# Optimization experiments

Measured on AMD Instinct MI355X. Metric: run time of the kernel, lower is better.

The kernel has to match this reference:

```python
import jax, jax.numpy as jnp
import numpy as np
from jax import lax

H = 1024  # hidden_size
L = 2     # num_layers


def gru_cell(x, h, Wih, Whh, bih, bhh):
    # PyTorch GRU gate order: r, z, n
    gi = x @ Wih.T + bih          # [B, 3H]
    gh = h @ Whh.T + bhh          # [B, 3H]
    ir, iz, inn = jnp.split(gi, 3, axis=-1)
    hr, hz, hn = jnp.split(gh, 3, axis=-1)
    r = jax.nn.sigmoid(ir + hr)
    z = jax.nn.sigmoid(iz + hz)
    n = jnp.tanh(inn + r * hn)
    return (1.0 - z) * n + z * h


def stacked_step(h, x_t, layers):
    # h: [L, B, H]; x_t: [B, in]; layers: list of (Wih, Whh, bih, bhh)
    hs = []
    inp = x_t
    for l, (Wih, Whh, bih, bhh) in enumerate(layers):
        hl = gru_cell(inp, h[l], Wih, Whh, bih, bhh)
        hs.append(hl)
        inp = hl
    return jnp.stack(hs), inp  # new hidden stack, top-layer output


def run_gru_seq(x_seq, h0, layers):
    # x_seq: [B, S, in] -> scan over time
    def step(h, x_t):
        h_new, out = stacked_step(h, x_t, layers)
        return h_new, out
    h_final, outs = lax.scan(step, h0, jnp.transpose(x_seq, (1, 0, 2)))
    return outs[-1], h_final  # last-timestep top-layer output [B, H]


def setup_inputs() -> dict:
    key = jax.random.key(0)
    ks = jax.random.split(key, 10)
    B, S = 128, 256

    def xavier(k, shape):
        fan_out, fan_in = shape
        std = np.sqrt(2.0 / (fan_in + fan_out))
        return jax.random.normal(k, shape, dtype=jnp.float32) * std

    inp = {
        "x": jax.random.normal(ks[0], (B, S), dtype=jnp.float32),
        "h0": jax.random.uniform(ks[1], (L, B, H), dtype=jnp.float32) * 0.01,
        "Wih0": xavier(ks[2], (3 * H, 1)),
        "Whh0": xavier(ks[3], (3 * H, H)),
        "bih0": jnp.zeros((3 * H,), jnp.float32),
        "bhh0": jnp.zeros((3 * H,), jnp.float32),
        "Wih1": xavier(ks[4], (3 * H, H)),
        "Whh1": xavier(ks[5], (3 * H, H)),
        "bih1": jnp.zeros((3 * H,), jnp.float32),
        "bhh1": jnp.zeros((3 * H,), jnp.float32),
        "fc_w": jax.random.uniform(ks[6], (1, H), jnp.float32, -1.0 / np.sqrt(H), 1.0 / np.sqrt(H)),
        "fc_b": jax.random.uniform(ks[7], (1,), jnp.float32, -1.0 / np.sqrt(H), 1.0 / np.sqrt(H)),
        "forcast_length": 8,
    }
    return inp


def reference(x, h0, Wih0, Whh0, bih0, bhh0, Wih1, Whh1, bih1, bhh1, fc_w, fc_b, forcast_length):
    layers = [(Wih0, Whh0, bih0, bhh0), (Wih1, Whh1, bih1, bhh1)]

    # forecast step i=0: full conditioning sequence
    out0, h = run_gru_seq(x[..., None], h0, layers)   # [B, H], [L, B, H]
    y0 = out0 @ fc_w.T + fc_b                          # [B, 1]

    def fstep(carry, _):
        xc, hc = carry                                 # xc: [B, 1]
        h_new, out = stacked_step(hc, xc, layers)
        y = out @ fc_w.T + fc_b                        # [B, 1]
        return (y, h_new), y[:, 0]

    (y_last, h_final), ys = lax.scan(fstep, (y0, h), None, length=forcast_length - 1)
    forcast_out = jnp.concatenate([y0[:, 0][None, :], ys], axis=0)  # [F, B]
    return jnp.mean(forcast_out, axis=0), h_final
```

## Files before the change

### kernel.cpp

```cpp
#include <hip/hip_runtime.h>

#define NB 128
#define NH 1024
#define NS 256
#define NF 8
#define NBLK 192
#define NTH 512
#define AG  __HIP_MEMORY_SCOPE_AGENT

#define GLOBL 0
#define RELL  64
#define INITL 128
#define XCNT  192
#define XARR  512
#define XCPY  1024

typedef _Float16 half_t;
typedef _Float16 f16x8 __attribute__((ext_vector_type(8)));
typedef float f32x4 __attribute__((ext_vector_type(4)));
typedef unsigned long long u64;

struct GP {
    const float *x, *hin, *Wih0, *Whh0, *bih0, *bhh0, *Wih1, *Whh1, *bih1, *bhh1, *fcw, *fcb;
    float *gib0, *gib1, *ypart, *out;
    half_t *h0b0, *h0b1, *h1b0, *h1b1;
    char *reg;
    unsigned *bar;
};

__device__ __forceinline__ float fast_sigmoid(float x) { return 1.0f / (1.0f + __expf(-x)); }
__device__ __forceinline__ float fast_tanh(float x) {
    float e = __expf(2.0f * x);
    return (e - 1.0f) / (e + 1.0f);
}

__device__ __forceinline__ u64 ldu64(const void* p) {
    return __hip_atomic_load((const u64*)p, __ATOMIC_RELAXED, AG);
}
__device__ __forceinline__ void stu64(void* p, u64 v) {
    __hip_atomic_store((u64*)p, v, __ATOMIC_RELAXED, AG);
}
__device__ __forceinline__ float ldf32(const float* p) {
    return __hip_atomic_load(p, __ATOMIC_RELAXED, AG);
}
__device__ __forceinline__ void stf32(float* p, float v) {
    __hip_atomic_store(p, v, __ATOMIC_RELAXED, AG);
}
__device__ __forceinline__ unsigned aadd(unsigned* p, unsigned v) {
    return __hip_atomic_fetch_add(p, v, __ATOMIC_RELAXED, AG);
}
__device__ __forceinline__ unsigned ald(const unsigned* p) {
    return __hip_atomic_load(p, __ATOMIC_RELAXED, AG);
}

__device__ __forceinline__ void l2add(unsigned* p, unsigned v) {
    asm volatile("global_atomic_add %0, %1, off" :: "v"(p), "v"(v) : "memory");
}
__device__ __forceinline__ unsigned l2add_rtn(unsigned* p, unsigned v) {
    unsigned ret;
    asm volatile("global_atomic_add %0, %1, %2, off sc0\n\ts_waitcnt vmcnt(0)"
                 : "=v"(ret) : "v"(p), "v"(v) : "memory");
    return ret;
}

__global__ void k_init(const float* __restrict__ hin, half_t* __restrict__ h0h,
                       half_t* __restrict__ h1h) {
    int i = blockIdx.x * 256 + threadIdx.x;
    h0h[i] = (half_t)hin[i];
    h1h[i] = (half_t)hin[NB * NH + i];
}

__global__ __launch_bounds__(NTH)
void k_gru(GP p) {
    extern __shared__ char lds[];
    const int tid = threadIdx.x;
    const int l   = tid & 63;
    const int wv  = tid >> 6;
    const int bid = blockIdx.x;
    const int role = (bid < 64) ? 0 : (bid < 128 ? 1 : 2);
    const int bc   = bid & 63;
    const int colbase = bc * 16;
    float* hl  = (float*)(lds + 98304);
    int* meta  = (int*)(lds + 106496);
    unsigned* bar = p.bar;

    {
        const float* Wsrc = (role == 0) ? p.Whh0 : ((role == 1) ? p.Wih1 : p.Whh1);
        for (int i = tid; i < 12288; i += NTH) {
            int row = i >> 8, j = i & 255;
            int g = row >> 4, r = row & 15;
            float4 v = *(const float4*)(Wsrc + (size_t)(g * NH + colbase + r) * NH + j * 4);
            union { half_t h[4]; uint2 u; } cv;
            cv.h[0] = (half_t)v.x; cv.h[1] = (half_t)v.y;
            cv.h[2] = (half_t)v.z; cv.h[3] = (half_t)v.w;
            *(uint2*)(lds + (row * 2048 + ((j * 8) ^ ((row & 7) << 4)))) = cv.u;
        }
        if (role != 1) {
            const float* hsrc = p.hin + (role == 2 ? NB * NH : 0);
            for (int i = tid; i < NB * 16; i += NTH) {
                int b = i >> 4, cl = i & 15;
                hl[i] = hsrc[(size_t)b * NH + colbase + cl];
            }
        }
    }

    if (tid == 0) {
        unsigned x;
        asm volatile("s_getreg_b32 %0, hwreg(HW_REG_XCC_ID)" : "=s"(x));
        x &= 7;
        unsigned r = aadd(bar + XCNT + x * 32, 1u);
        asm volatile("s_waitcnt vmcnt(0)" ::: "memory");
        aadd(bar + INITL, 1u);
        while (ald(bar + INITL) < NBLK) __builtin_amdgcn_s_sleep(1);
        int nn = 0, cnt = 0;
        for (int k = 0; k < 8; ++k) {
            unsigned c = ald(bar + XCNT + k * 32);
            if (c) ++cnt;
            if (k == (int)x) nn = (int)c;
        }
        meta[0] = (int)x; meta[1] = (int)r; meta[2] = nn; meta[3] = cnt;
    }
    __syncthreads();
    const int xcd_  = meta[0];
    const int rank_ = meta[1];
    const int n_    = meta[2];
    const int nx_   = meta[3];

    const int cloc = l & 15;
    const int c = colbase + cloc;
    float bi_[3] = {0,0,0}, bh_[3] = {0,0,0}, wx_[3] = {0,0,0}, fcwv = 0.f, fcb_ = 0.f;
    if (role == 0) {
        #pragma unroll
        for (int g = 0; g < 3; ++g) {
            bi_[g] = p.bih0[g * NH + c]; bh_[g] = p.bhh0[g * NH + c];
            wx_[g] = p.Wih0[g * NH + c];
        }
        fcb_ = p.fcb[0];
    } else if (role == 2) {
        #pragma unroll
        for (int g = 0; g < 3; ++g) {
            bi_[g] = p.bih1[g * NH + c]; bh_[g] = p.bhh1[g * NH + c];
        }
        fcwv = p.fcw[c];
    }

    const int rbase[3] = { cloc * 2048, (16 + cloc) * 2048, (32 + cloc) * 2048 };
    const int rmask = (cloc & 7) << 4;
    const int kb0 = (l >> 4) << 4;
    const int arow = wv * 16 + cloc;
    const int b0base = wv * 16 + ((l >> 4) << 2);
    const int aloff = (l >> 4) * 2048 + arow * 16;

    auto gbar = [&](unsigned t) {
        __syncthreads();
        if (tid == 0) {
            l2add(bar + XARR + xcd_ * 32, 1u);
            if (rank_ == 0) {
                while (l2add_rtn(bar + XARR + xcd_ * 32, 0u) < (unsigned)n_ * t)
                    __builtin_amdgcn_s_sleep(1);
                unsigned old = aadd(bar + GLOBL, 1u);
                if (old == (unsigned)nx_ * t - 1u) aadd(bar + RELL, 1u);
            }
            while (ald(bar + RELL) < t) __builtin_amdgcn_s_sleep(1);
        }
        __syncthreads();
        asm volatile("buffer_inv" ::: "memory");
    };

    auto xcopy = [&](const half_t* h0s, const half_t* h1s, int slot) {
        char* dst = p.reg + ((size_t)(xcd_ * 2 + slot)) * 524288;
        for (int idx = rank_ * NTH + tid; idx < 32768; idx += n_ * NTH) {
            int which = idx >> 14, kq = (idx >> 7) & 127, row = idx & 127;
            const half_t* s = (which ? h1s : h0s) + row * 1024 + kq * 8;
            union { u64 u[2]; uint4 v; } t;
            t.u[0] = ldu64(s);
            t.u[1] = ldu64(s + 4);
            *(uint4*)(dst + which * 262144 + (size_t)(kq * 128 + row) * 16) = t.v;
        }
    };
    auto csync = [&](unsigned ct) {
        __syncthreads();
        if (tid == 0) {
            l2add(bar + XCPY + xcd_ * 32, 1u);
            while (l2add_rtn(bar + XCPY + xcd_ * 32, 0u) < (unsigned)n_ * ct)
                __builtin_amdgcn_s_sleep(1);
        }
        __syncthreads();
    };

    auto do_gemm = [&](const char* regA, f32x4 (&acc)[3]) {
        const char* ap = regA + aloff;
        #pragma unroll 16
        for (int ks = 0; ks < 32; ++ks) {
            f16x8 a = *(const f16x8*)(ap + (size_t)ks * 8192);
            int kb = ks * 64 + kb0;
            #pragma unroll
            for (int g = 0; g < 3; ++g) {
                f16x8 bf = *(const f16x8*)(lds + rbase[g] + (kb ^ rmask));
                acc[g] = __builtin_amdgcn_mfma_f32_16x16x32_f16(a, bf, acc[g], 0, 0, 0);
            }
        }
    };

    auto pack_store_h = [&](half_t* hw, int b, float hn) {
        unsigned v = (unsigned)__builtin_bit_cast(unsigned short, (half_t)hn);
        unsigned o = __shfl_xor(v, 1);
        unsigned pair = (l & 1) ? (o | (v << 16)) : (v | (o << 16));
        unsigned p2 = __shfl_xor(pair, 2);
        u64 quad = (l & 2) ? (((u64)pair << 32) | p2) : ((u64)pair | ((u64)p2 << 32));
        if ((l & 3) == 0) stu64(hw + (size_t)b * NH + (c & ~3), quad);
    };

    auto l0_epi = [&](const float xv[4], f32x4 (&acc)[3], half_t* hw) {
        #pragma unroll
        for (int q = 0; q < 4; ++q) {
            int b = b0base + q;
            float gh0 = acc[0][q] + bh_[0];
            float gh1 = acc[1][q] + bh_[1];
            float gh2 = acc[2][q] + bh_[2];
            float r_ = fast_sigmoid(xv[q] * wx_[0] + bi_[0] + gh0);
            float z_ = fast_sigmoid(xv[q] * wx_[1] + bi_[1] + gh1);
            float n_2 = fast_tanh(xv[q] * wx_[2] + bi_[2] + r_ * gh2);
            float hp = hl[b * 16 + cloc];
            float hn = (1.0f - z_) * n_2 + z_ * hp;
            hl[b * 16 + cloc] = hn;
            pack_store_h(hw, b, hn);
        }
    };

    auto gi_epi = [&](f32x4 (&acc)[3], float* gw) {
        #pragma unroll
        for (int g = 0; g < 3; ++g) {
            union { f32x4 v; u64 u[2]; } t; t.v = acc[g];
            float* dst = gw + ((size_t)g * NH + c) * NB + b0base;
            stu64(dst, t.u[0]);
            stu64(dst + 2, t.u[1]);
        }
    };

    auto gh_epi = [&](f32x4 (&acc)[3], const f32x4 gv[3], half_t* hw, float* ydst) {
        float hn4[4];
        #pragma unroll
        for (int q = 0; q < 4; ++q) {
            int b = b0base + q;
            float gh0 = acc[0][q] + bh_[0];
            float gh1 = acc[1][q] + bh_[1];
            float gh2 = acc[2][q] + bh_[2];
            float r_ = fast_sigmoid(gv[0][q] + bi_[0] + gh0);
            float z_ = fast_sigmoid(gv[1][q] + bi_[1] + gh1);
            float n_2 = fast_tanh(gv[2][q] + bi_[2] + r_ * gh2);
            float hp = hl[b * 16 + cloc];
            float hn = (1.0f - z_) * n_2 + z_ * hp;
            hl[b * 16 + cloc] = hn;
            hn4[q] = hn;
            pack_store_h(hw, b, hn);
        }
        if (ydst) {
            float s0 = hn4[0] * fcwv, s1 = hn4[1] * fcwv, s2 = hn4[2] * fcwv, s3 = hn4[3] * fcwv;
            #pragma unroll
            for (int m = 1; m < 16; m <<= 1) {
                s0 += __shfl_xor(s0, m); s1 += __shfl_xor(s1, m);
                s2 += __shfl_xor(s2, m); s3 += __shfl_xor(s3, m);
            }
            if (cloc == 0) {
                float* yp = ydst + bc * NB + b0base;
                stf32(yp,     s0);
                stf32(yp + 1, s1);
                stf32(yp + 2, s2);
                stf32(yp + 3, s3);
            }
        }
    };

    auto load_gi = [&](const float* gr, f32x4 (&gv)[3]) {
        #pragma unroll
        for (int g = 0; g < 3; ++g) {
            union { f32x4 v; u64 u[2]; } t;
            const float* src = gr + ((size_t)g * NH + c) * NB + b0base;
            t.u[0] = ldu64(src);
            t.u[1] = ldu64(src + 2);
            gv[g] = t.v;
        }
    };

    auto reduce_y = [&](float xv[4]) {
        float s[4];
        #pragma unroll
        for (int q = 0; q < 4; ++q) {
            float t0 = ldf32(p.ypart + (cloc * 4 + 0) * NB + b0base + q);
            float t1 = ldf32(p.ypart + (cloc * 4 + 1) * NB + b0base + q);
            float t2 = ldf32(p.ypart + (cloc * 4 + 2) * NB + b0base + q);
            float t3 = ldf32(p.ypart + (cloc * 4 + 3) * NB + b0base + q);
            s[q] = (t0 + t1) + (t2 + t3);
        }
        #pragma unroll
        for (int m = 1; m < 16; m <<= 1) {
            s[0] += __shfl_xor(s[0], m); s[1] += __shfl_xor(s[1], m);
            s[2] += __shfl_xor(s[2], m); s[3] += __shfl_xor(s[3], m);
        }
        #pragma unroll
        for (int q = 0; q < 4; ++q) xv[q] = s[q] + fcb_;
    };

    unsigned tgt = 0, ctgt = 0;
    int cur0 = 0, cur1 = 0, gcur = 0;
    f32x4 zero4 = {0.f, 0.f, 0.f, 0.f};
    float ysum[4] = {0.f, 0.f, 0.f, 0.f};

    auto COPY = [&]() {
        ++ctgt;
        int slot = (int)(ctgt & 1);
        xcopy(cur0 ? p.h0b1 : p.h0b0, cur1 ? p.h1b1 : p.h1b0, slot);
        csync(ctgt);
        return (const char*)(p.reg + (size_t)(xcd_ * 2 + slot) * 524288);
    };

    for (int ph = 0; ph < NS + 2; ++ph) {
        float xv[4];
        f32x4 gv[3];
        if (role == 0 && ph < NS) {
            #pragma unroll
            for (int q = 0; q < 4; ++q) xv[q] = p.x[(size_t)(b0base + q) * NS + ph];
        } else if (role == 2 && ph >= 2) {
            load_gi(gcur ? p.gib1 : p.gib0, gv);
        }
        const char* regB = COPY();
        if (role == 0 && ph < NS) {
            f32x4 acc[3] = {zero4, zero4, zero4};
            do_gemm(regB, acc);
            l0_epi(xv, acc, cur0 ? p.h0b0 : p.h0b1);
        } else if (role == 1 && ph >= 1 && ph <= NS) {
            f32x4 acc[3] = {zero4, zero4, zero4};
            do_gemm(regB, acc);
            gi_epi(acc, gcur ? p.gib0 : p.gib1);
        } else if (role == 2 && ph >= 2) {
            f32x4 acc[3] = {zero4, zero4, zero4};
            do_gemm(regB + 262144, acc);
            gh_epi(acc, gv, cur1 ? p.h1b0 : p.h1b1, (ph == NS + 1) ? p.ypart : nullptr);
        }
        ++tgt; gbar(tgt);
        if (ph < NS) cur0 ^= 1;
        if (ph >= 1 && ph <= NS) gcur ^= 1;
        if (ph >= 2) cur1 ^= 1;
    }

    for (int i = 1; i < NF; ++i) {
        float xv[4];
        if (role == 0) {
            reduce_y(xv);
            #pragma unroll
            for (int q = 0; q < 4; ++q) ysum[q] += xv[q];
        }
        const char* regB = COPY();
        if (role == 0) {
            f32x4 acc[3] = {zero4, zero4, zero4};
            do_gemm(regB, acc);
            l0_epi(xv, acc, cur0 ? p.h0b0 : p.h0b1);
        }
        ++tgt; gbar(tgt); cur0 ^= 1;

        regB = COPY();
        if (role == 1) {
            f32x4 acc[3] = {zero4, zero4, zero4};
            do_gemm(regB, acc);
            gi_epi(acc, gcur ? p.gib0 : p.gib1);
        }
        ++tgt; gbar(tgt); gcur ^= 1;

        {
            f32x4 gv[3];
            if (role == 2) load_gi(gcur ? p.gib1 : p.gib0, gv);
            regB = COPY();
            if (role == 2) {
                f32x4 acc[3] = {zero4, zero4, zero4};
                do_gemm(regB + 262144, acc);
                gh_epi(acc, gv, cur1 ? p.h1b0 : p.h1b1, p.ypart);
            }
        }
        ++tgt; gbar(tgt); cur1 ^= 1;
    }

    if (role == 0) {
        float y7[4];
        reduce_y(y7);
        if (bid == 0 && cloc == 0) {
            #pragma unroll
            for (int q = 0; q < 4; ++q)
                p.out[b0base + q] = (ysum[q] + y7[q]) * 0.125f;
        }
    }
    if (role != 1) {
        float* ob = p.out + NB + (role == 2 ? (size_t)NB * NH : 0);
        for (int i = tid; i < NB * 16; i += NTH) {
            int b = i >> 4, cl = i & 15;
            ob[(size_t)b * NH + colbase + cl] = hl[i];
        }
    }
}

extern "C" void kernel_launch(void* const* d_in, const int* in_sizes, int n_in,
                              void* d_out, int out_size, void* d_ws, size_t ws_size,
                              hipStream_t stream)
{
    GP p;
    p.x    = (const float*)d_in[0];
    p.hin  = (const float*)d_in[1];
    p.Wih0 = (const float*)d_in[2];
    p.Whh0 = (const float*)d_in[3];
    p.bih0 = (const float*)d_in[4];
    p.bhh0 = (const float*)d_in[5];
    p.Wih1 = (const float*)d_in[6];
    p.Whh1 = (const float*)d_in[7];
    p.bih1 = (const float*)d_in[8];
    p.bhh1 = (const float*)d_in[9];
    p.fcw  = (const float*)d_in[10];
    p.fcb  = (const float*)d_in[11];
    p.out  = (float*)d_out;

    char* ws = (char*)d_ws;
    p.bar   = (unsigned*)ws;                     ws += 8192;
    p.h0b0  = (half_t*)ws;                       ws += 262144;
    p.h0b1  = (half_t*)ws;                       ws += 262144;
    p.h1b0  = (half_t*)ws;                       ws += 262144;
    p.h1b1  = (half_t*)ws;                       ws += 262144;
    p.gib0  = (float*)ws;                        ws += 1572864;
    p.gib1  = (float*)ws;                        ws += 1572864;
    p.ypart = (float*)ws;                        ws += 32768;
    ws = (char*)(((size_t)ws + 4095) & ~(size_t)4095);
    p.reg   = ws;                                ws += 8 * 2 * 524288;

    hipMemsetAsync(p.bar, 0, 8192, stream);
    k_init<<<512, 256, 0, stream>>>(p.hin, p.h0b0, p.h1b0);

    void* args[] = { &p };
    if (hipLaunchCooperativeKernel((void*)k_gru, dim3(NBLK), dim3(NTH), args,
                                   106752, stream) != hipSuccess) {
        (void)hipGetLastError();
        k_gru<<<dim3(NBLK), dim3(NTH), 106752, stream>>>(p);
    }
}
```

Before: 3.721 ms.

## Fuse layer-1 input and hidden GEMMs into one role, drop gi buffers

Replaces the separate layer-1 input-projection blocks and hidden-projection blocks with a single role of 128 blocks, each owning 8 columns and computing both Wih1·h0 and Whh1·h1 from LDS-resident weights. The gi global round-trip goes away, and so does a grid barrier per forecast step. The main pipeline shortens from NS+2 phases to NS+1. Gates are computed across lane pairs using shuffles, and the y partial reduction now sums 128 partials instead of 64. In exchange, each layer-1 block does four MFMA chains per k-step and reads two A operands, and unroll depth is reduced.

Result: slower. 3.844 ms (+3.3%).

```diff
diff --git a/kernel.cpp b/kernel.cpp
--- a/kernel.cpp
+++ b/kernel.cpp
@@ -22,7 +22,7 @@
 
 struct GP {
     const float *x, *hin, *Wih0, *Whh0, *bih0, *bhh0, *Wih1, *Whh1, *bih1, *bhh1, *fcw, *fcb;
-    float *gib0, *gib1, *ypart, *out;
+    float *ypart, *out;
     half_t *h0b0, *h0b1, *h1b0, *h1b1;
     char *reg;
     unsigned *bar;
@@ -77,30 +77,41 @@
     const int l   = tid & 63;
     const int wv  = tid >> 6;
     const int bid = blockIdx.x;
-    const int role = (bid < 64) ? 0 : (bid < 128 ? 1 : 2);
-    const int bc   = bid & 63;
-    const int colbase = bc * 16;
+    const int role = (bid < 64) ? 0 : 1;
+    const int lc   = bid - 64;
+    const int colbase = role ? lc * 8 : bid * 16;
     float* hl  = (float*)(lds + 98304);
     int* meta  = (int*)(lds + 106496);
     unsigned* bar = p.bar;
 
+    const int cloc = l & 15;
+    const int col8 = cloc & 7;
+
     {
-        const float* Wsrc = (role == 0) ? p.Whh0 : ((role == 1) ? p.Wih1 : p.Whh1);
         for (int i = tid; i < 12288; i += NTH) {
             int row = i >> 8, j = i & 255;
-            int g = row >> 4, r = row & 15;
-            float4 v = *(const float4*)(Wsrc + (size_t)(g * NH + colbase + r) * NH + j * 4);
+            const float* Wsrc;
+            int wrow;
+            if (role == 0) {
+                Wsrc = p.Whh0; wrow = (row >> 4) * NH + colbase + (row & 15);
+            } else {
+                int plane = row >> 3, cl = row & 7;
+                Wsrc = (plane < 3) ? p.Wih1 : p.Whh1;
+                int g = (plane < 3) ? plane : plane - 3;
+                wrow = g * NH + colbase + cl;
+            }
+            float4 v = *(const float4*)(Wsrc + (size_t)wrow * NH + j * 4);
             union { half_t h[4]; uint2 u; } cv;
             cv.h[0] = (half_t)v.x; cv.h[1] = (half_t)v.y;
             cv.h[2] = (half_t)v.z; cv.h[3] = (half_t)v.w;
             *(uint2*)(lds + (row * 2048 + ((j * 8) ^ ((row & 7) << 4)))) = cv.u;
         }
-        if (role != 1) {
-            const float* hsrc = p.hin + (role == 2 ? NB * NH : 0);
-            for (int i = tid; i < NB * 16; i += NTH) {
-                int b = i >> 4, cl = i & 15;
-                hl[i] = hsrc[(size_t)b * NH + colbase + cl];
-            }
+        if (role == 0) {
+            for (int i = tid; i < NB * 16; i += NTH)
+                hl[i] = p.hin[(size_t)(i >> 4) * NH + colbase + (i & 15)];
+        } else {
+            for (int i = tid; i < NB * 8; i += NTH)
+                hl[i] = p.hin[(size_t)NB * NH + (size_t)(i >> 3) * NH + colbase + (i & 7)];
         }
     }
 
@@ -126,26 +137,27 @@
     const int n_    = meta[2];
     const int nx_   = meta[3];
 
-    const int cloc = l & 15;
-    const int c = colbase + cloc;
     float bi_[3] = {0,0,0}, bh_[3] = {0,0,0}, wx_[3] = {0,0,0}, fcwv = 0.f, fcb_ = 0.f;
+    float bi_lo = 0.f, bh_lo = 0.f, bi2 = 0.f, bh2 = 0.f;
     if (role == 0) {
+        int c = colbase + cloc;
         #pragma unroll
         for (int g = 0; g < 3; ++g) {
             bi_[g] = p.bih0[g * NH + c]; bh_[g] = p.bhh0[g * NH + c];
             wx_[g] = p.Wih0[g * NH + c];
         }
         fcb_ = p.fcb[0];
-    } else if (role == 2) {
-        #pragma unroll
-        for (int g = 0; g < 3; ++g) {
-            bi_[g] = p.bih1[g * NH + c]; bh_[g] = p.bhh1[g * NH + c];
-        }
-        fcwv = p.fcw[c];
-    }
-
-    const int rbase[3] = { cloc * 2048, (16 + cloc) * 2048, (32 + cloc) * 2048 };
-    const int rmask = (cloc & 7) << 4;
+    } else {
+        int glo = cloc >> 3;
+        int c8 = colbase + col8;
+        bi_lo = p.bih1[glo * NH + c8]; bh_lo = p.bhh1[glo * NH + c8];
+        bi2   = p.bih1[2 * NH + c8];   bh2   = p.bhh1[2 * NH + c8];
+        fcwv  = p.fcw[c8];
+    }
+
+    const int rb_l0[3] = { cloc * 2048, (16 + cloc) * 2048, (32 + cloc) * 2048 };
+    const int rb_l1[4] = { cloc * 2048, (16 + col8) * 2048, (24 + cloc) * 2048, (40 + col8) * 2048 };
+    const int rmask = (col8) << 4;
     const int kb0 = (l >> 4) << 4;
     const int arow = wv * 16 + cloc;
     const int b0base = wv * 16 + ((l >> 4) << 2);
@@ -188,27 +200,46 @@
         __syncthreads();
     };
 
-    auto do_gemm = [&](const char* regA, f32x4 (&acc)[3]) {
+    auto gemm_l0 = [&](const char* regA, f32x4 (&acc)[3]) {
         const char* ap = regA + aloff;
-        #pragma unroll 16
+        #pragma unroll 8
         for (int ks = 0; ks < 32; ++ks) {
             f16x8 a = *(const f16x8*)(ap + (size_t)ks * 8192);
             int kb = ks * 64 + kb0;
             #pragma unroll
             for (int g = 0; g < 3; ++g) {
-                f16x8 bf = *(const f16x8*)(lds + rbase[g] + (kb ^ rmask));
+                f16x8 bf = *(const f16x8*)(lds + rb_l0[g] + (kb ^ rmask));
                 acc[g] = __builtin_amdgcn_mfma_f32_16x16x32_f16(a, bf, acc[g], 0, 0, 0);
             }
         }
     };
 
-    auto pack_store_h = [&](half_t* hw, int b, float hn) {
+    auto gemm_l1 = [&](const char* regA, f32x4 (&acc)[4]) {
+        const char* ap0 = regA + aloff;
+        const char* ap1 = regA + 262144 + aloff;
+        #pragma unroll 8
+        for (int ks = 0; ks < 32; ++ks) {
+            f16x8 a0 = *(const f16x8*)(ap0 + (size_t)ks * 8192);
+            f16x8 a1 = *(const f16x8*)(ap1 + (size_t)ks * 8192);
+            int kb = ks * 64 + kb0;
+            f16x8 b0 = *(const f16x8*)(lds + rb_l1[0] + (kb ^ rmask));
+            acc[0] = __builtin_amdgcn_mfma_f32_16x16x32_f16(a0, b0, acc[0], 0, 0, 0);
+            f16x8 b1 = *(const f16x8*)(lds + rb_l1[1] + (kb ^ rmask));
+            acc[1] = __builtin_amdgcn_mfma_f32_16x16x32_f16(a0, b1, acc[1], 0, 0, 0);
+            f16x8 b2 = *(const f16x8*)(lds + rb_l1[2] + (kb ^ rmask));
+            acc[2] = __builtin_amdgcn_mfma_f32_16x16x32_f16(a1, b2, acc[2], 0, 0, 0);
+            f16x8 b3 = *(const f16x8*)(lds + rb_l1[3] + (kb ^ rmask));
+            acc[3] = __builtin_amdgcn_mfma_f32_16x16x32_f16(a1, b3, acc[3], 0, 0, 0);
+        }
+    };
+
+    auto pack_store16 = [&](half_t* hw, int b, float hn) {
         unsigned v = (unsigned)__builtin_bit_cast(unsigned short, (half_t)hn);
         unsigned o = __shfl_xor(v, 1);
         unsigned pair = (l & 1) ? (o | (v << 16)) : (v | (o << 16));
         unsigned p2 = __shfl_xor(pair, 2);
         u64 quad = (l & 2) ? (((u64)pair << 32) | p2) : ((u64)pair | ((u64)p2 << 32));
-        if ((l & 3) == 0) stu64(hw + (size_t)b * NH + (c & ~3), quad);
+        if ((l & 3) == 0) stu64(hw + (size_t)b * NH + ((colbase + cloc) & ~3), quad);
     };
 
     auto l0_epi = [&](const float xv[4], f32x4 (&acc)[3], half_t* hw) {
@@ -224,86 +255,62 @@
             float hp = hl[b * 16 + cloc];
             float hn = (1.0f - z_) * n_2 + z_ * hp;
             hl[b * 16 + cloc] = hn;
-            pack_store_h(hw, b, hn);
-        }
-    };
-
-    auto gi_epi = [&](f32x4 (&acc)[3], float* gw) {
-        #pragma unroll
-        for (int g = 0; g < 3; ++g) {
-            union { f32x4 v; u64 u[2]; } t; t.v = acc[g];
-            float* dst = gw + ((size_t)g * NH + c) * NB + b0base;
-            stu64(dst, t.u[0]);
-            stu64(dst + 2, t.u[1]);
-        }
-    };
-
-    auto gh_epi = [&](f32x4 (&acc)[3], const f32x4 gv[3], half_t* hw, float* ydst) {
-        float hn4[4];
+            pack_store16(hw, b, hn);
+        }
+    };
+
+    auto l1_epi = [&](f32x4 (&acc)[4], half_t* hw, float* ydst) {
         #pragma unroll
         for (int q = 0; q < 4; ++q) {
             int b = b0base + q;
-            float gh0 = acc[0][q] + bh_[0];
-            float gh1 = acc[1][q] + bh_[1];
-            float gh2 = acc[2][q] + bh_[2];
-            float r_ = fast_sigmoid(gv[0][q] + bi_[0] + gh0);
-            float z_ = fast_sigmoid(gv[1][q] + bi_[1] + gh1);
-            float n_2 = fast_tanh(gv[2][q] + bi_[2] + r_ * gh2);
-            float hp = hl[b * 16 + cloc];
-            float hn = (1.0f - z_) * n_2 + z_ * hp;
-            hl[b * 16 + cloc] = hn;
-            hn4[q] = hn;
-            pack_store_h(hw, b, hn);
-        }
-        if (ydst) {
-            float s0 = hn4[0] * fcwv, s1 = hn4[1] * fcwv, s2 = hn4[2] * fcwv, s3 = hn4[3] * fcwv;
-            #pragma unroll
-            for (int m = 1; m < 16; m <<= 1) {
-                s0 += __shfl_xor(s0, m); s1 += __shfl_xor(s1, m);
-                s2 += __shfl_xor(s2, m); s3 += __shfl_xor(s3, m);
+            float rz = fast_sigmoid(acc[0][q] + bi_lo + acc[2][q] + bh_lo);
+            float zv = __shfl_xor(rz, 8);
+            float n_2 = fast_tanh(acc[1][q] + bi2 + rz * (acc[3][q] + bh2));
+            float hp = hl[b * 8 + col8];
+            float hn = (1.0f - zv) * n_2 + zv * hp;
+            if (cloc < 8) hl[b * 8 + col8] = hn;
+            unsigned v = (unsigned)__builtin_bit_cast(unsigned short, (half_t)hn);
+            unsigned o = __shfl_xor(v, 1);
+            unsigned pair = (l & 1) ? (o | (v << 16)) : (v | (o << 16));
+            unsigned p2 = __shfl_xor(pair, 2);
+            u64 quad = (l & 2) ? (((u64)pair << 32) | p2) : ((u64)pair | ((u64)p2 << 32));
+            if ((l & 3) == 0 && cloc < 8)
+                stu64(hw + (size_t)b * NH + ((colbase + col8) & ~3), quad);
+            if (ydst) {
+                float s = hn * fcwv;
+                s += __shfl_xor(s, 1);
+                s += __shfl_xor(s, 2);
+                s += __shfl_xor(s, 4);
+                if (cloc == 0) stf32(ydst + lc * NB + b, s);
             }
-            if (cloc == 0) {
-                float* yp = ydst + bc * NB + b0base;
-                stf32(yp,     s0);
-                stf32(yp + 1, s1);
-                stf32(yp + 2, s2);
-                stf32(yp + 3, s3);
-            }
-        }
-    };
-
-    auto load_gi = [&](const float* gr, f32x4 (&gv)[3]) {
-        #pragma unroll
-        for (int g = 0; g < 3; ++g) {
-            union { f32x4 v; u64 u[2]; } t;
-            const float* src = gr + ((size_t)g * NH + c) * NB + b0base;
-            t.u[0] = ldu64(src);
-            t.u[1] = ldu64(src + 2);
-            gv[g] = t.v;
         }
     };
 
     auto reduce_y = [&](float xv[4]) {
-        float s[4];
         #pragma unroll
         for (int q = 0; q < 4; ++q) {
-            float t0 = ldf32(p.ypart + (cloc * 4 + 0) * NB + b0base + q);
-            float t1 = ldf32(p.ypart + (cloc * 4 + 1) * NB + b0base + q);
-            float t2 = ldf32(p.ypart + (cloc * 4 + 2) * NB + b0base + q);
-            float t3 = ldf32(p.ypart + (cloc * 4 + 3) * NB + b0base + q);
-            s[q] = (t0 + t1) + (t2 + t3);
+            int b = b0base + q;
+            float t0 = ldf32(p.ypart + (cloc * 8 + 0) * NB + b);
+            float t1 = ldf32(p.ypart + (cloc * 8 + 1) * NB + b);
+            float t2 = ldf32(p.ypart + (cloc * 8 + 2) * NB + b);
+            float t3 = ldf32(p.ypart + (cloc * 8 + 3) * NB + b);
+            float t4 = ldf32(p.ypart + (cloc * 8 + 4) * NB + b);
+            float t5 = ldf32(p.ypart + (cloc * 8 + 5) * NB + b);
+            float t6 = ldf32(p.ypart + (cloc * 8 + 6) * NB + b);
+            float t7 = ldf32(p.ypart + (cloc * 8 + 7) * NB + b);
+            xv[q] = ((t0 + t1) + (t2 + t3)) + ((t4 + t5) + (t6 + t7));
         }
         #pragma unroll
         for (int m = 1; m < 16; m <<= 1) {
-            s[0] += __shfl_xor(s[0], m); s[1] += __shfl_xor(s[1], m);
-            s[2] += __shfl_xor(s[2], m); s[3] += __shfl_xor(s[3], m);
-        }
-        #pragma unroll
-        for (int q = 0; q < 4; ++q) xv[q] = s[q] + fcb_;
+            xv[0] += __shfl_xor(xv[0], m); xv[1] += __shfl_xor(xv[1], m);
+            xv[2] += __shfl_xor(xv[2], m); xv[3] += __shfl_xor(xv[3], m);
+        }
+        #pragma unroll
+        for (int q = 0; q < 4; ++q) xv[q] += fcb_;
     };
 
     unsigned tgt = 0, ctgt = 0;
-    int cur0 = 0, cur1 = 0, gcur = 0;
+    int cur0 = 0, cur1 = 0;
     f32x4 zero4 = {0.f, 0.f, 0.f, 0.f};
     float ysum[4] = {0.f, 0.f, 0.f, 0.f};
 
@@ -315,33 +322,25 @@
         return (const char*)(p.reg + (size_t)(xcd_ * 2 + slot) * 524288);
     };
 
-    for (int ph = 0; ph < NS + 2; ++ph) {
+    for (int ph = 0; ph <= NS; ++ph) {
         float xv[4];
-        f32x4 gv[3];
         if (role == 0 && ph < NS) {
             #pragma unroll
             for (int q = 0; q < 4; ++q) xv[q] = p.x[(size_t)(b0base + q) * NS + ph];
-        } else if (role == 2 && ph >= 2) {
-            load_gi(gcur ? p.gib1 : p.gib0, gv);
         }
         const char* regB = COPY();
         if (role == 0 && ph < NS) {
             f32x4 acc[3] = {zero4, zero4, zero4};
-            do_gemm(regB, acc);
+            gemm_l0(regB, acc);
             l0_epi(xv, acc, cur0 ? p.h0b0 : p.h0b1);
-        } else if (role == 1 && ph >= 1 && ph <= NS) {
-            f32x4 acc[3] = {zero4, zero4, zero4};
-            do_gemm(regB, acc);
-            gi_epi(acc, gcur ? p.gib0 : p.gib1);
-        } else if (role == 2 && ph >= 2) {
-            f32x4 acc[3] = {zero4, zero4, zero4};
-            do_gemm(regB + 262144, acc);
-            gh_epi(acc, gv, cur1 ? p.h1b0 : p.h1b1, (ph == NS + 1) ? p.ypart : nullptr);
+        } else if (role == 1 && ph >= 1) {
+            f32x4 acc[4] = {zero4, zero4, zero4, zero4};
+            gemm_l1(regB, acc);
+            l1_epi(acc, cur1 ? p.h1b0 : p.h1b1, (ph == NS) ? p.ypart : nullptr);
         }
         ++tgt; gbar(tgt);
         if (ph < NS) cur0 ^= 1;
-        if (ph >= 1 && ph <= NS) gcur ^= 1;
-        if (ph >= 2) cur1 ^= 1;
+        if (ph >= 1) cur1 ^= 1;
     }
 
     for (int i = 1; i < NF; ++i) {
@@ -354,28 +353,16 @@
         const char* regB = COPY();
         if (role == 0) {
             f32x4 acc[3] = {zero4, zero4, zero4};
-            do_gemm(regB, acc);
+            gemm_l0(regB, acc);
             l0_epi(xv, acc, cur0 ? p.h0b0 : p.h0b1);
         }
         ++tgt; gbar(tgt); cur0 ^= 1;
 
         regB = COPY();
         if (role == 1) {
-            f32x4 acc[3] = {zero4, zero4, zero4};
-            do_gemm(regB, acc);
-            gi_epi(acc, gcur ? p.gib0 : p.gib1);
-        }
-        ++tgt; gbar(tgt); gcur ^= 1;
-
-        {
-            f32x4 gv[3];
-            if (role == 2) load_gi(gcur ? p.gib1 : p.gib0, gv);
-            regB = COPY();
-            if (role == 2) {
-                f32x4 acc[3] = {zero4, zero4, zero4};
-                do_gemm(regB + 262144, acc);
-                gh_epi(acc, gv, cur1 ? p.h1b0 : p.h1b1, p.ypart);
-            }
+            f32x4 acc[4] = {zero4, zero4, zero4, zero4};
+            gemm_l1(regB, acc);
+            l1_epi(acc, cur1 ? p.h1b0 : p.h1b1, p.ypart);
         }
         ++tgt; gbar(tgt); cur1 ^= 1;
     }
@@ -388,13 +375,13 @@
             for (int q = 0; q < 4; ++q)
                 p.out[b0base + q] = (ysum[q] + y7[q]) * 0.125f;
         }
-    }
-    if (role != 1) {
-        float* ob = p.out + NB + (role == 2 ? (size_t)NB * NH : 0);
-        for (int i = tid; i < NB * 16; i += NTH) {
-            int b = i >> 4, cl = i & 15;
-            ob[(size_t)b * NH + colbase + cl] = hl[i];
-        }
+        float* ob = p.out + NB;
+        for (int i = tid; i < NB * 16; i += NTH)
+            ob[(size_t)(i >> 4) * NH + colbase + (i & 15)] = hl[i];
+    } else {
+        float* ob = p.out + NB + (size_t)NB * NH;
+        for (int i = tid; i < NB * 8; i += NTH)
+            ob[(size_t)(i >> 3) * NH + colbase + (i & 7)] = hl[i];
     }
 }
 
@@ -423,9 +410,7 @@
     p.h0b1  = (half_t*)ws;                       ws += 262144;
     p.h1b0  = (half_t*)ws;                       ws += 262144;
     p.h1b1  = (half_t*)ws;                       ws += 262144;
-    p.gib0  = (float*)ws;                        ws += 1572864;
-    p.gib1  = (float*)ws;                        ws += 1572864;
-    p.ypart = (float*)ws;                        ws += 32768;
+    p.ypart = (float*)ws;                        ws += 65536;
     ws = (char*)(((size_t)ws + 4095) & ~(size_t)4095);
     p.reg   = ws;                                ws += 8 * 2 * 524288;
 
```
